# Performance work log

Hardware: AMD Instinct MI355X
Metric: run time of the kernel (lower is better)

Reference implementation:

```python
import jax, jax.numpy as jnp
import numpy as np

HEADS = 8
NEG_SLOPE = 0.2  # PyG GATConv default LeakyReLU slope


def _gat_layer(x, src, dst, W, a_src, a_dst, bias, heads, out_ch):
    """PyG-style GATConv (concat heads, self-loops already appended, eval mode).
    x: [N, F_in]; src/dst: [E_tot] int; W: [F_in, heads*out_ch];
    a_src/a_dst: [heads, out_ch]; bias: [heads*out_ch].
    """
    N = x.shape[0]
    h = (x @ W).reshape(N, heads, out_ch)                      # [N, H, C]
    # per-node attention logits (gathered per edge as scalars, not features)
    al_s = jnp.einsum('nhc,hc->nh', h, a_src)                  # [N, H]
    al_d = jnp.einsum('nhc,hc->nh', h, a_dst)                  # [N, H]
    e = jax.nn.leaky_relu(al_s[src] + al_d[dst], negative_slope=NEG_SLOPE)  # [E, H]
    # segment softmax over incoming edges of each target node (stable)
    e_max = jax.ops.segment_max(e, dst, num_segments=N)        # self-loops => no empty segments
    ex = jnp.exp(e - e_max[dst])
    denom = jax.ops.segment_sum(ex, dst, num_segments=N)
    alpha = ex / (denom[dst] + 1e-16)                          # [E, H]
    # gather source features, weight, scatter-add to targets
    out = jax.ops.segment_sum(h[src] * alpha[:, :, None], dst, num_segments=N)  # [N, H, C]
    return out.reshape(N, heads * out_ch) + bias


def setup_inputs() -> dict:
    key = jax.random.key(0)
    ks = jax.random.split(key, 16)
    N, E, F_IN, NUM_CLASSES = 50000, 1600000, 128, 16
    s = 0.1
    return {
        'x': jax.random.normal(ks[0], (N, F_IN), dtype=jnp.float32),
        'edge_index': jax.random.randint(ks[1], (2, E), 0, N, dtype=jnp.int64),
        # GAT layer 1: 128 -> 8 heads x 8
        'W1': jax.random.normal(ks[2], (F_IN, 64), dtype=jnp.float32) * s,
        'a1_src': jax.random.normal(ks[3], (8, 8), dtype=jnp.float32) * s,
        'a1_dst': jax.random.normal(ks[4], (8, 8), dtype=jnp.float32) * s,
        'b1': jnp.zeros((64,), dtype=jnp.float32),
        # GAT layer 2: 64 -> 8 heads x 4
        'W2': jax.random.normal(ks[5], (64, 32), dtype=jnp.float32) * s,
        'a2_src': jax.random.normal(ks[6], (8, 4), dtype=jnp.float32) * s,
        'a2_dst': jax.random.normal(ks[7], (8, 4), dtype=jnp.float32) * s,
        'b2': jnp.zeros((32,), dtype=jnp.float32),
        # torch MultiheadAttention(32, 8): packed in_proj [96,32], out_proj [32,32]
        'in_proj_w': jax.random.normal(ks[8], (96, 32), dtype=jnp.float32) * s,
        'in_proj_b': jnp.zeros((96,), dtype=jnp.float32),
        'out_proj_w': jax.random.normal(ks[9], (32, 32), dtype=jnp.float32) * s,
        'out_proj_b': jnp.zeros((32,), dtype=jnp.float32),
        # fc: 32 -> num_classes
        'fc_w': jax.random.normal(ks[10], (NUM_CLASSES, 32), dtype=jnp.float32) * s,
        'fc_b': jnp.zeros((NUM_CLASSES,), dtype=jnp.float32),
    }


def reference(x, edge_index, W1, a1_src, a1_dst, b1, W2, a2_src, a2_dst, b2,
              in_proj_w, in_proj_b, out_proj_w, out_proj_b, fc_w, fc_b):
    N = x.shape[0]
    loops = jnp.arange(N, dtype=edge_index.dtype)
    src = jnp.concatenate([edge_index[0], loops])  # PyG add_self_loops=True
    dst = jnp.concatenate([edge_index[1], loops])

    h = jax.nn.elu(_gat_layer(x, src, dst, W1, a1_src, a1_dst, b1, HEADS, 8))   # [N, 64]
    h = jax.nn.elu(_gat_layer(h, src, dst, W2, a2_src, a2_dst, b2, HEADS, 4))   # [N, 32]

    # MultiheadAttention on h.unsqueeze(0): shape [1, N, 32] with torch's
    # seq-first layout => seq_len = 1, batch = N. Softmax over a single key
    # is identically 1 for every head, so out = out_proj(v_proj(h)).
    v = h @ in_proj_w[64:96].T + in_proj_b[64:96]   # v-projection slice of packed in_proj
    h = v @ out_proj_w.T + out_proj_b               # [N, 32]

    logits = h @ fc_w.T + fc_b                      # [N, num_classes]
    return jax.nn.log_softmax(logits, axis=1)
```

## Files before the change

### kernel.cpp

```cpp
#include <hip/hip_runtime.h>
#include <hip/hip_bf16.h>
#include <math.h>


#define BSHIFT 7
#define BMASK  ((1 << BSHIFT) - 1)
#define MAXNB  512
#define TILE   8192
#define XST    136

typedef __attribute__((ext_vector_type(8))) short short8;
typedef __attribute__((ext_vector_type(4))) float floatx4;
typedef __attribute__((ext_vector_type(2))) float floatx2;

__device__ __forceinline__ unsigned short f2bf(float f) {
    union { float f; unsigned int u; } v; v.f = f;
    unsigned int u = v.u;
    return (unsigned short)((u + 0x7FFFu + ((u >> 16) & 1u)) >> 16);
}
__device__ __forceinline__ float lrelu(float e) { return fmaxf(e, 0.2f * e); }
__device__ __forceinline__ float elu(float o) {
    return (o > 0.f) ? o : (__expf(o) - 1.f);
}

__global__ __launch_bounds__(256) void bin_scatter1_kernel(
    const int* __restrict__ ei, int E, int Et, int NB, int CAP,
    int* __restrict__ gcount, unsigned int* __restrict__ rec) {
    __shared__ int h[MAXNB];
    __shared__ int cur[MAXNB];
    for (int i = threadIdx.x; i < NB; i += 256) h[i] = 0;
    __syncthreads();
    int tile0 = blockIdx.x * TILE;
    int jend = tile0 + TILE; if (jend > Et) jend = Et;
    for (int j = tile0 + threadIdx.x; j < jend; j += 256) {
        int d = (j < E) ? ei[E + j] : (j - E);
        atomicAdd(&h[d >> BSHIFT], 1);
    }
    __syncthreads();
    for (int i = threadIdx.x; i < NB; i += 256)
        cur[i] = h[i] ? atomicAdd(&gcount[i], h[i]) : 0;
    __syncthreads();
    for (int j = tile0 + threadIdx.x; j < jend; j += 256) {
        int srcv, d;
        if (j < E) { srcv = ei[j]; d = ei[E + j]; } else { srcv = j - E; d = j - E; }
        int b = d >> BSHIFT;
        int pos = atomicAdd(&cur[b], 1);
        if (pos < CAP)
            rec[(size_t)b * CAP + pos] = (unsigned)srcv | ((unsigned)(d & BMASK) << 16);
    }
}

__global__ __launch_bounds__(512) void scan_fold_kernel(
    const int* __restrict__ gcount, int* __restrict__ bbase, int NB, int CAP,
    const float* __restrict__ in_proj_w, const float* __restrict__ in_proj_b,
    const float* __restrict__ out_proj_w, const float* __restrict__ out_proj_b,
    const float* __restrict__ fc_w, const float* __restrict__ fc_b,
    float* __restrict__ M, float* __restrict__ bf) {
    __shared__ int s[512];
    __shared__ float Wvo[32 * 32];
    __shared__ float bvo[32];
    int t = threadIdx.x;
    if (blockIdx.x == 0) {
        int v = 0;
        if (t < NB) { v = gcount[t]; if (v > CAP) v = CAP; }
        s[t] = v;
        __syncthreads();
        for (int off = 1; off < 512; off <<= 1) {
            int u = (t >= off) ? s[t - off] : 0;
            __syncthreads();
            s[t] += u;
            __syncthreads();
        }
        if (t < NB) bbase[t] = s[t] - v;
    } else {
        const float* Wv = in_proj_w + 64 * 32;
        const float* bv = in_proj_b + 64;
        for (int idx = t; idx < 1024; idx += 512) {
            int i = idx >> 5, j = idx & 31;
            float acc = 0.f;
            for (int k = 0; k < 32; ++k) acc += out_proj_w[i * 32 + k] * Wv[k * 32 + j];
            Wvo[idx] = acc;
        }
        if (t < 32) {
            float acc = 0.f;
            for (int k = 0; k < 32; ++k) acc += out_proj_w[t * 32 + k] * bv[k];
            bvo[t] = acc + out_proj_b[t];
        }
        __syncthreads();
        for (int idx = t; idx < 16 * 32; idx += 512) {
            int cc = idx >> 5, j = idx & 31;
            float acc = 0.f;
            for (int i = 0; i < 32; ++i) acc += fc_w[cc * 32 + i] * Wvo[i * 32 + j];
            M[idx] = acc;
        }
        if (t < 16) {
            float acc = 0.f;
            for (int i = 0; i < 32; ++i) acc += fc_w[t * 32 + i] * bvo[i];
            bf[t] = acc + fc_b[t];
        }
    }
}

__global__ __launch_bounds__(256) void csr_finalize_kernel(
    const unsigned int* __restrict__ rec, const int* __restrict__ gcount,
    const int* __restrict__ bbase, int* __restrict__ rowp,
    unsigned short* __restrict__ esrc, int N, int Et, int CAP) {
    __shared__ int h[128];
    __shared__ int nb[128];
    __shared__ int cur[128];
    int b = blockIdx.x, t = threadIdx.x;
    size_t rbase = (size_t)b * CAP;
    int cnt = gcount[b]; if (cnt > CAP) cnt = CAP;
    int obase = bbase[b];
    if (t < 128) h[t] = 0;
    __syncthreads();
    for (int i = t; i < cnt; i += 256)
        atomicAdd(&h[(rec[rbase + i] >> 16) & 127], 1);
    __syncthreads();
    if (t == 0) {
        int run = obase;
        for (int i = 0; i < 128; ++i) { nb[i] = run; run += h[i]; }
    }
    __syncthreads();
    if (t < 128) cur[t] = nb[t];
    int n0 = b << BSHIFT;
    if (t < 128 && n0 + t < N) rowp[n0 + t] = nb[t];
    if (b == 0 && t == 0) rowp[N] = Et;
    __syncthreads();
    for (int i = t; i < cnt; i += 256) {
        unsigned r = rec[rbase + i];
        int pos = atomicAdd(&cur[(r >> 16) & 127], 1);
        esrc[pos] = (unsigned short)(r & 0xFFFFu);
    }
}

__global__ __launch_bounds__(256) void gemm1_mfma_kernel(
    const float* __restrict__ x, const float* __restrict__ W,
    const float* __restrict__ a_src, const float* __restrict__ a_dst,
    char* __restrict__ rec1, float* __restrict__ ald, int N) {
    __shared__ __align__(16) unsigned short xs[64 * XST];
    __shared__ __align__(16) unsigned short wt[64 * XST];
    int t = threadIdx.x;
    int nb = blockIdx.x * 64;
#pragma unroll
    for (int r = 0; r < 8; ++r) {
        int p = t + 256 * r;
        int row = p >> 5;
        int c4  = p & 31;
        int n = nb + row;
        float4 v = (n < N) ? ((const float4*)x)[(size_t)n * 32 + c4]
                           : make_float4(0.f, 0.f, 0.f, 0.f);
        unsigned short* dst = &xs[row * XST + c4 * 4];
        dst[0] = f2bf(v.x); dst[1] = f2bf(v.y);
        dst[2] = f2bf(v.z); dst[3] = f2bf(v.w);
    }
    {
        int n = t & 63, kg = t >> 6;
#pragma unroll
        for (int c = 0; c < 4; ++c) {
            int k0 = kg * 32 + c * 8;
            unsigned short* dst = &wt[n * XST + k0];
#pragma unroll
            for (int j = 0; j < 8; ++j)
                dst[j] = f2bf(W[(k0 + j) * 64 + n]);
        }
    }
    __syncthreads();
    int wave = t >> 6, lane = t & 63;
    int m16 = lane & 15, quad = lane >> 4;
    floatx4 acc[4];
#pragma unroll
    for (int i = 0; i < 4; ++i) acc[i] = (floatx4){0.f, 0.f, 0.f, 0.f};
#pragma unroll
    for (int k = 0; k < 4; ++k) {
        int koff = k * 32 + quad * 8;
        short8 afrag = *(const short8*)&xs[(wave * 16 + m16) * XST + koff];
#pragma unroll
        for (int nt = 0; nt < 4; ++nt) {
            short8 bfrag = *(const short8*)&wt[(nt * 16 + m16) * XST + koff];
            acc[nt] = __builtin_amdgcn_mfma_f32_16x16x32_bf16(afrag, bfrag, acc[nt], 0, 0, 0);
        }
    }
    __syncthreads();
    float* hs = (float*)xs;
#pragma unroll
    for (int nt = 0; nt < 4; ++nt)
#pragma unroll
        for (int r = 0; r < 4; ++r)
            hs[(wave * 16 + quad * 4 + r) * 65 + nt * 16 + m16] = acc[nt][r];
    __syncthreads();
    float asv = a_src[lane], adv = a_dst[lane];
    for (int itn = 0; itn < 16; ++itn) {
        int nl = wave * 16 + itn;
        int n = nb + nl;
        if (n >= N) break;
        float v = hs[nl * 65 + lane];
        float ps = v * asv, pd = v * adv;
        ps += __shfl_xor(ps, 1); ps += __shfl_xor(ps, 2); ps += __shfl_xor(ps, 4);
        pd += __shfl_xor(pd, 1); pd += __shfl_xor(pd, 2); pd += __shfl_xor(pd, 4);
        if ((lane & 7) == 0) {
            *(float*)(rec1 + (size_t)n * 96 + 4 * (lane >> 3)) = ps;
            ald[n * 8 + (lane >> 3)] = pd;
        }
        if (lane < 16) {
            const float* hr = &hs[nl * 65 + lane * 4];
            int pk = __builtin_amdgcn_cvt_pk_fp8_f32(hr[0], hr[1], 0, false);
            pk = __builtin_amdgcn_cvt_pk_fp8_f32(hr[2], hr[3], pk, true);
            *(unsigned*)(rec1 + (size_t)n * 96 + 32 + 4 * lane) = (unsigned)pk;
        }
    }
}

__global__ __launch_bounds__(256) void gat_agg64_g2_kernel(
    const int* __restrict__ rowp, const unsigned short* __restrict__ esrc,
    const char* __restrict__ rec1, const float* __restrict__ ald_arr,
    const float* __restrict__ bias,
    const float* __restrict__ W2, const float* __restrict__ a2s,
    const float* __restrict__ a2d,
    char* __restrict__ rec2, float* __restrict__ ald2, int N) {
    __shared__ __align__(16) float W2p[2][8][32][4];
    __shared__ __align__(16) float oL[4][64];
    __shared__ __align__(16) float h2L[4][32];
    int t = threadIdx.x;
    for (int idx = t; idx < 2048; idx += 256) {
        int k = idx >> 5, l = idx & 31;
        W2p[k >> 5][(k & 31) >> 2][l][k & 3] = W2[idx];
    }
    __syncthreads();
    const int lane = t & 63;
    const int wv = t >> 6;
    const int e = lane >> 4;
    const int c = lane & 15;
    const int hd = c >> 1;
    const int aoff = 4 * hd;
    const int foff = 32 + 4 * c;
    int n = blockIdx.x * 4 + wv;
    if (n >= N) return;
    float aldv = ald_arr[n * 8 + hd];
    int beg = rowp[n], end = rowp[n + 1];
    float dA = 0.f, dB = 0.f;
    floatx2 p0a = {0.f, 0.f}, p0b = {0.f, 0.f};
    floatx2 p1a = {0.f, 0.f}, p1b = {0.f, 0.f};
    floatx2 p2a = {0.f, 0.f}, p2b = {0.f, 0.f};
    floatx2 p3a = {0.f, 0.f}, p3b = {0.f, 0.f};
    int i = beg;
    int s0, s1, s2, s3;
    bool has = (i + 16 <= end);
    if (has) {
        s0 = esrc[i + e]; s1 = esrc[i + 4 + e];
        s2 = esrc[i + 8 + e]; s3 = esrc[i + 12 + e];
    }
    while (has) {
        int t0 = s0, t1 = s1, t2 = s2, t3 = s3;
        i += 16;
        has = (i + 16 <= end);
        if (has) {
            s0 = esrc[i + e]; s1 = esrc[i + 4 + e];
            s2 = esrc[i + 8 + e]; s3 = esrc[i + 12 + e];
        }
        const char* r0 = rec1 + (size_t)t0 * 96;
        const char* r1 = rec1 + (size_t)t1 * 96;
        const char* r2 = rec1 + (size_t)t2 * 96;
        const char* r3 = rec1 + (size_t)t3 * 96;
        float e0 = *(const float*)(r0 + aoff) + aldv;
        float e1 = *(const float*)(r1 + aoff) + aldv;
        float e2 = *(const float*)(r2 + aoff) + aldv;
        float e3 = *(const float*)(r3 + aoff) + aldv;
        unsigned g0 = *(const unsigned*)(r0 + foff);
        unsigned g1 = *(const unsigned*)(r1 + foff);
        unsigned g2 = *(const unsigned*)(r2 + foff);
        unsigned g3 = *(const unsigned*)(r3 + foff);
        float w0 = __expf(lrelu(e0));
        float w1 = __expf(lrelu(e1));
        float w2 = __expf(lrelu(e2));
        float w3 = __expf(lrelu(e3));
        dA += w0; dB += w1; dA += w2; dB += w3;
        p0a += w0 * __builtin_amdgcn_cvt_pk_f32_fp8(g0, false);
        p0b += w0 * __builtin_amdgcn_cvt_pk_f32_fp8(g0, true);
        p1a += w1 * __builtin_amdgcn_cvt_pk_f32_fp8(g1, false);
        p1b += w1 * __builtin_amdgcn_cvt_pk_f32_fp8(g1, true);
        p2a += w2 * __builtin_amdgcn_cvt_pk_f32_fp8(g2, false);
        p2b += w2 * __builtin_amdgcn_cvt_pk_f32_fp8(g2, true);
        p3a += w3 * __builtin_amdgcn_cvt_pk_f32_fp8(g3, false);
        p3b += w3 * __builtin_amdgcn_cvt_pk_f32_fp8(g3, true);
    }
    for (; i < end; i += 4) {
        int rem = end - i;
        int ee = (e < rem) ? e : rem - 1;
        int s = esrc[i + ee];
        const char* r = rec1 + (size_t)s * 96;
        float ev = *(const float*)(r + aoff) + aldv;
        unsigned g = *(const unsigned*)(r + foff);
        float w = (e < rem) ? __expf(lrelu(ev)) : 0.f;
        dA += w;
        p0a += w * __builtin_amdgcn_cvt_pk_f32_fp8(g, false);
        p0b += w * __builtin_amdgcn_cvt_pk_f32_fp8(g, true);
    }
    float d = dA + dB;
    floatx2 Pa = (p0a + p1a) + (p2a + p3a);
    floatx2 Pb = (p0b + p1b) + (p2b + p3b);
    float P0 = Pa.x, P1 = Pa.y, P2 = Pb.x, P3 = Pb.y;
    d  += __shfl_xor(d, 16);  d  += __shfl_xor(d, 32);
    P0 += __shfl_xor(P0, 16); P0 += __shfl_xor(P0, 32);
    P1 += __shfl_xor(P1, 16); P1 += __shfl_xor(P1, 32);
    P2 += __shfl_xor(P2, 16); P2 += __shfl_xor(P2, 32);
    P3 += __shfl_xor(P3, 16); P3 += __shfl_xor(P3, 32);
    float inv = 1.f / (d + 1e-16f);
    float4 bv = ((const float4*)bias)[c];
    float o0 = elu(P0 * inv + bv.x);
    float o1 = elu(P1 * inv + bv.y);
    float o2 = elu(P2 * inv + bv.z);
    float o3 = elu(P3 * inv + bv.w);
    if (lane < 16) *(float4*)&oL[wv][c * 4] = make_float4(o0, o1, o2, o3);
    const int l = lane & 31, kh = lane >> 5;
    const float* orow = &oL[wv][kh * 32];
    float a0 = 0.f, a1 = 0.f, a2 = 0.f, a3 = 0.f;
#pragma unroll
    for (int g = 0; g < 8; ++g) {
        float4 ov = *(const float4*)&orow[g * 4];
        float4 wv4 = *(const float4*)&W2p[kh][g][l][0];
        a0 += ov.x * wv4.x; a1 += ov.y * wv4.y;
        a2 += ov.z * wv4.z; a3 += ov.w * wv4.w;
    }
    float acc = (a0 + a1) + (a2 + a3);
    acc += __shfl_xor(acc, 32);
    float ps = acc * a2s[l], pd = acc * a2d[l];
    ps += __shfl_xor(ps, 1); ps += __shfl_xor(ps, 2);
    pd += __shfl_xor(pd, 1); pd += __shfl_xor(pd, 2);
    if (lane < 32) {
        h2L[wv][l] = acc;
        if ((l & 3) == 0) {
            *(float*)(rec2 + (size_t)n * 64 + 4 * (l >> 2)) = ps;
            ald2[n * 8 + (l >> 2)] = pd;
        }
    }
    if (lane < 8) {
        const float* hr = &h2L[wv][lane * 4];
        int pk = __builtin_amdgcn_cvt_pk_fp8_f32(hr[0], hr[1], 0, false);
        pk = __builtin_amdgcn_cvt_pk_fp8_f32(hr[2], hr[3], pk, true);
        *(unsigned*)(rec2 + (size_t)n * 64 + 32 + 4 * lane) = (unsigned)pk;
    }
}

__global__ __launch_bounds__(256) void gat_agg32_fin_kernel(
    const int* __restrict__ rowp, const unsigned short* __restrict__ esrc,
    const char* __restrict__ rec2, const float* __restrict__ ald_arr,
    const float* __restrict__ bias,
    const float* __restrict__ M, const float* __restrict__ bf,
    float* __restrict__ out, int N) {
    __shared__ __align__(16) float Mp[8][16][4];
    __shared__ float bfs[16];
    __shared__ __align__(16) float oL[4][32];
    int t = threadIdx.x;
    for (int i = t; i < 512; i += 256) {
        int j = i >> 5, k = i & 31;
        Mp[k >> 2][j][k & 3] = M[i];
    }
    if (t < 16) bfs[t] = bf[t];
    __syncthreads();
    const int lane = t & 63;
    const int wv = t >> 6;
    const int e = lane >> 3;
    const int c = lane & 7;
    const int aoff = 4 * c;
    const int foff = 32 + 4 * c;
    int n = blockIdx.x * 4 + wv;
    if (n >= N) return;
    float aldv = ald_arr[n * 8 + c];
    int beg = rowp[n], end = rowp[n + 1];
    float d0 = 0.f, d1 = 0.f, d2 = 0.f, d3 = 0.f;
    floatx2 p0a = {0.f, 0.f}, p0b = {0.f, 0.f};
    floatx2 p1a = {0.f, 0.f}, p1b = {0.f, 0.f};
    floatx2 p2a = {0.f, 0.f}, p2b = {0.f, 0.f};
    floatx2 p3a = {0.f, 0.f}, p3b = {0.f, 0.f};
    for (int base = beg; base < end; base += 32) {
        int i0 = base + e;
        int i1 = base + 8 + e;
        int i2 = base + 16 + e;
        int i3 = base + 24 + e;
        bool v0 = i0 < end, v1 = i1 < end, v2 = i2 < end, v3 = i3 < end;
        int c0 = v0 ? i0 : beg;
        int c1 = v1 ? i1 : beg;
        int c2 = v2 ? i2 : beg;
        int c3 = v3 ? i3 : beg;
        int s0 = esrc[c0], s1 = esrc[c1], s2 = esrc[c2], s3 = esrc[c3];
        const char* r0 = rec2 + (size_t)s0 * 64;
        const char* r1 = rec2 + (size_t)s1 * 64;
        const char* r2 = rec2 + (size_t)s2 * 64;
        const char* r3 = rec2 + (size_t)s3 * 64;
        float e0 = *(const float*)(r0 + aoff) + aldv;
        float e1 = *(const float*)(r1 + aoff) + aldv;
        float e2 = *(const float*)(r2 + aoff) + aldv;
        float e3 = *(const float*)(r3 + aoff) + aldv;
        unsigned g0 = *(const unsigned*)(r0 + foff);
        unsigned g1 = *(const unsigned*)(r1 + foff);
        unsigned g2 = *(const unsigned*)(r2 + foff);
        unsigned g3 = *(const unsigned*)(r3 + foff);
        float w0 = v0 ? __expf(lrelu(e0)) : 0.f;
        float w1 = v1 ? __expf(lrelu(e1)) : 0.f;
        float w2 = v2 ? __expf(lrelu(e2)) : 0.f;
        float w3 = v3 ? __expf(lrelu(e3)) : 0.f;
        d0 += w0; d1 += w1; d2 += w2; d3 += w3;
        p0a += w0 * __builtin_amdgcn_cvt_pk_f32_fp8(g0, false);
        p0b += w0 * __builtin_amdgcn_cvt_pk_f32_fp8(g0, true);
        p1a += w1 * __builtin_amdgcn_cvt_pk_f32_fp8(g1, false);
        p1b += w1 * __builtin_amdgcn_cvt_pk_f32_fp8(g1, true);
        p2a += w2 * __builtin_amdgcn_cvt_pk_f32_fp8(g2, false);
        p2b += w2 * __builtin_amdgcn_cvt_pk_f32_fp8(g2, true);
        p3a += w3 * __builtin_amdgcn_cvt_pk_f32_fp8(g3, false);
        p3b += w3 * __builtin_amdgcn_cvt_pk_f32_fp8(g3, true);
    }
    float d = (d0 + d1) + (d2 + d3);
    floatx2 Pa = (p0a + p1a) + (p2a + p3a);
    floatx2 Pb = (p0b + p1b) + (p2b + p3b);
    float P0 = Pa.x, P1 = Pa.y, P2 = Pb.x, P3 = Pb.y;
    d  += __shfl_xor(d, 8);  d  += __shfl_xor(d, 16);  d  += __shfl_xor(d, 32);
    P0 += __shfl_xor(P0, 8); P0 += __shfl_xor(P0, 16); P0 += __shfl_xor(P0, 32);
    P1 += __shfl_xor(P1, 8); P1 += __shfl_xor(P1, 16); P1 += __shfl_xor(P1, 32);
    P2 += __shfl_xor(P2, 8); P2 += __shfl_xor(P2, 16); P2 += __shfl_xor(P2, 32);
    P3 += __shfl_xor(P3, 8); P3 += __shfl_xor(P3, 16); P3 += __shfl_xor(P3, 32);
    float inv = 1.f / (d + 1e-16f);
    float4 bv = ((const float4*)bias)[c];
    float o0 = elu(P0 * inv + bv.x);
    float o1 = elu(P1 * inv + bv.y);
    float o2 = elu(P2 * inv + bv.z);
    float o3 = elu(P3 * inv + bv.w);
    if (lane < 8) *(float4*)&oL[wv][c * 4] = make_float4(o0, o1, o2, o3);
    const int j = lane & 15;
    const float* orow = oL[wv];
    float a0 = 0.f, a1 = 0.f, a2 = 0.f, a3 = 0.f;
#pragma unroll
    for (int g = 0; g < 8; ++g) {
        float4 ov = *(const float4*)&orow[g * 4];
        float4 mv = *(const float4*)&Mp[g][j][0];
        a0 += ov.x * mv.x; a1 += ov.y * mv.y;
        a2 += ov.z * mv.z; a3 += ov.w * mv.w;
    }
    float logit = (a0 + a1) + (a2 + a3) + bfs[j];
    float mx = logit;
    mx = fmaxf(mx, __shfl_xor(mx, 1));
    mx = fmaxf(mx, __shfl_xor(mx, 2));
    mx = fmaxf(mx, __shfl_xor(mx, 4));
    mx = fmaxf(mx, __shfl_xor(mx, 8));
    float ex = __expf(logit - mx);
    float se = ex;
    se += __shfl_xor(se, 1);
    se += __shfl_xor(se, 2);
    se += __shfl_xor(se, 4);
    se += __shfl_xor(se, 8);
    float res = logit - (mx + __logf(se));
    if (lane < 16) out[(size_t)n * 16 + j] = res;
}

extern "C" void kernel_launch(void* const* d_in, const int* in_sizes, int n_in,
                              void* d_out, int out_size, void* d_ws, size_t ws_size,
                              hipStream_t stream) {
    const float* x   = (const float*)d_in[0];
    const int*   ei  = (const int*)d_in[1];
    const float* W1  = (const float*)d_in[2];
    const float* a1s = (const float*)d_in[3];
    const float* a1d = (const float*)d_in[4];
    const float* b1  = (const float*)d_in[5];
    const float* W2  = (const float*)d_in[6];
    const float* a2s = (const float*)d_in[7];
    const float* a2d = (const float*)d_in[8];
    const float* b2  = (const float*)d_in[9];
    const float* ipw = (const float*)d_in[10];
    const float* ipb = (const float*)d_in[11];
    const float* opw = (const float*)d_in[12];
    const float* opb = (const float*)d_in[13];
    const float* fcw = (const float*)d_in[14];
    const float* fcb = (const float*)d_in[15];
    float* out = (float*)d_out;

    int N = in_sizes[0] / 128;
    int E = in_sizes[1] / 2;
    int Et = E + N;
    int NB = (N + BMASK) >> BSHIFT;
    int NTILES = (Et + TILE - 1) / TILE;
    int CAP = Et / NB;
    CAP = CAP + CAP / 8 + 256;
    CAP = (CAP + 255) & ~255;

    char* ws = (char*)d_ws;
    size_t off = 0;
    auto alloc = [&](size_t bytes) -> void* {
        void* p = ws + off;
        off += bytes;
        off = (off + 255) & ~(size_t)255;
        return p;
    };
    int*   bcount = (int*)alloc(MAXNB * 4);
    int*   bbase  = (int*)alloc(MAXNB * 4);
    unsigned int*   rec  = (unsigned int*)alloc((size_t)NB * CAP * 4);
    int*   rowp   = (int*)alloc((size_t)(N + 1) * 4);
    unsigned short* esrc = (unsigned short*)alloc((size_t)Et * 2);
    char* rec1   = (char*)alloc((size_t)N * 96);
    float* al1d  = (float*)alloc((size_t)N * 8 * 4);
    char* rec2   = (char*)alloc((size_t)N * 64);
    float* al2d  = (float*)alloc((size_t)N * 8 * 4);
    float* Mf    = (float*)alloc(512 * 4);
    float* bff   = (float*)alloc(16 * 4);
    (void)ws_size; (void)n_in; (void)out_size;

    hipMemsetAsync(bcount, 0, MAXNB * 4, stream);
    bin_scatter1_kernel<<<NTILES, 256, 0, stream>>>(ei, E, Et, NB, CAP, bcount, rec);
    scan_fold_kernel<<<2, 512, 0, stream>>>(bcount, bbase, NB, CAP,
                                            ipw, ipb, opw, opb, fcw, fcb, Mf, bff);
    csr_finalize_kernel<<<NB, 256, 0, stream>>>(rec, bcount, bbase, rowp, esrc, N, Et, CAP);

    gemm1_mfma_kernel<<<(N + 63) / 64, 256, 0, stream>>>(x, W1, a1s, a1d, rec1, al1d, N);
    gat_agg64_g2_kernel<<<(N + 3) / 4, 256, 0, stream>>>(
        rowp, esrc, rec1, al1d, b1, W2, a2s, a2d, rec2, al2d, N);
    gat_agg32_fin_kernel<<<(N + 3) / 4, 256, 0, stream>>>(
        rowp, esrc, rec2, al2d, b2, Mf, bff, out, N);
}
```

Baseline: 238.2 us.

## Stage edges in LDS, split layer-1 records, unroll aggregation loops

The binning kernel now caches each tile's packed (src,dst) edges in shared memory, so the second pass no longer rereads edge_index from global memory. Layer-1 per-node data is split from one 96-byte record into separate fp8 feature and source-logit arrays. The layer-1 aggregation loop is unrolled to 8 edges per lane with a masked tail, replacing the software-pipelined 4-edge loop. Layer-2 aggregation gains a mask-free fast path for full 32-edge chunks. The split layout reads two cache lines per gathered source instead of one, which may add memory traffic.

```diff
diff --git a/kernel.cpp b/kernel.cpp
--- a/kernel.cpp
+++ b/kernel.cpp
@@ -26,27 +26,32 @@
 __global__ __launch_bounds__(256) void bin_scatter1_kernel(
     const int* __restrict__ ei, int E, int Et, int NB, int CAP,
     int* __restrict__ gcount, unsigned int* __restrict__ rec) {
+    __shared__ unsigned int lrec[TILE];
     __shared__ int h[MAXNB];
     __shared__ int cur[MAXNB];
-    for (int i = threadIdx.x; i < NB; i += 256) h[i] = 0;
-    __syncthreads();
+    int t = threadIdx.x;
+    for (int i = t; i < NB; i += 256) h[i] = 0;
     int tile0 = blockIdx.x * TILE;
-    int jend = tile0 + TILE; if (jend > Et) jend = Et;
-    for (int j = tile0 + threadIdx.x; j < jend; j += 256) {
-        int d = (j < E) ? ei[E + j] : (j - E);
+    int cnt = Et - tile0; if (cnt > TILE) cnt = TILE;
+    __syncthreads();
+    for (int j = t; j < cnt; j += 256) {
+        int jj = tile0 + j;
+        int srcv, d;
+        if (jj < E) { srcv = ei[jj]; d = ei[E + jj]; } else { srcv = jj - E; d = jj - E; }
+        lrec[j] = (unsigned)srcv | ((unsigned)d << 16);
         atomicAdd(&h[d >> BSHIFT], 1);
     }
     __syncthreads();
-    for (int i = threadIdx.x; i < NB; i += 256)
+    for (int i = t; i < NB; i += 256)
         cur[i] = h[i] ? atomicAdd(&gcount[i], h[i]) : 0;
     __syncthreads();
-    for (int j = tile0 + threadIdx.x; j < jend; j += 256) {
-        int srcv, d;
-        if (j < E) { srcv = ei[j]; d = ei[E + j]; } else { srcv = j - E; d = j - E; }
-        int b = d >> BSHIFT;
+    for (int j = t; j < cnt; j += 256) {
+        unsigned v = lrec[j];
+        int b = v >> (16 + BSHIFT);
         int pos = atomicAdd(&cur[b], 1);
         if (pos < CAP)
-            rec[(size_t)b * CAP + pos] = (unsigned)srcv | ((unsigned)(d & BMASK) << 16);
+            rec[(size_t)b * CAP + pos] =
+                (v & 0xFFFFu) | ((((v >> 16) & BMASK)) << 16);
     }
 }
 
@@ -137,7 +142,8 @@
 __global__ __launch_bounds__(256) void gemm1_mfma_kernel(
     const float* __restrict__ x, const float* __restrict__ W,
     const float* __restrict__ a_src, const float* __restrict__ a_dst,
-    char* __restrict__ rec1, float* __restrict__ ald, int N) {
+    unsigned int* __restrict__ h1p, float* __restrict__ als,
+    float* __restrict__ ald, int N) {
     __shared__ __align__(16) unsigned short xs[64 * XST];
     __shared__ __align__(16) unsigned short wt[64 * XST];
     int t = threadIdx.x;
@@ -199,22 +205,22 @@
         ps += __shfl_xor(ps, 1); ps += __shfl_xor(ps, 2); ps += __shfl_xor(ps, 4);
         pd += __shfl_xor(pd, 1); pd += __shfl_xor(pd, 2); pd += __shfl_xor(pd, 4);
         if ((lane & 7) == 0) {
-            *(float*)(rec1 + (size_t)n * 96 + 4 * (lane >> 3)) = ps;
+            als[n * 8 + (lane >> 3)] = ps;
             ald[n * 8 + (lane >> 3)] = pd;
         }
         if (lane < 16) {
             const float* hr = &hs[nl * 65 + lane * 4];
             int pk = __builtin_amdgcn_cvt_pk_fp8_f32(hr[0], hr[1], 0, false);
             pk = __builtin_amdgcn_cvt_pk_fp8_f32(hr[2], hr[3], pk, true);
-            *(unsigned*)(rec1 + (size_t)n * 96 + 32 + 4 * lane) = (unsigned)pk;
+            h1p[(size_t)n * 16 + lane] = (unsigned)pk;
         }
     }
 }
 
 __global__ __launch_bounds__(256) void gat_agg64_g2_kernel(
     const int* __restrict__ rowp, const unsigned short* __restrict__ esrc,
-    const char* __restrict__ rec1, const float* __restrict__ ald_arr,
-    const float* __restrict__ bias,
+    const unsigned int* __restrict__ feat, const float* __restrict__ als,
+    const float* __restrict__ ald_arr, const float* __restrict__ bias,
     const float* __restrict__ W2, const float* __restrict__ a2s,
     const float* __restrict__ a2d,
     char* __restrict__ rec2, float* __restrict__ ald2, int N) {
@@ -232,8 +238,6 @@
     const int e = lane >> 4;
     const int c = lane & 15;
     const int hd = c >> 1;
-    const int aoff = 4 * hd;
-    const int foff = 32 + 4 * c;
     int n = blockIdx.x * 4 + wv;
     if (n >= N) return;
     float aldv = ald_arr[n * 8 + hd];
@@ -244,37 +248,29 @@
     floatx2 p2a = {0.f, 0.f}, p2b = {0.f, 0.f};
     floatx2 p3a = {0.f, 0.f}, p3b = {0.f, 0.f};
     int i = beg;
-    int s0, s1, s2, s3;
-    bool has = (i + 16 <= end);
-    if (has) {
-        s0 = esrc[i + e]; s1 = esrc[i + 4 + e];
-        s2 = esrc[i + 8 + e]; s3 = esrc[i + 12 + e];
-    }
-    while (has) {
-        int t0 = s0, t1 = s1, t2 = s2, t3 = s3;
-        i += 16;
-        has = (i + 16 <= end);
-        if (has) {
-            s0 = esrc[i + e]; s1 = esrc[i + 4 + e];
-            s2 = esrc[i + 8 + e]; s3 = esrc[i + 12 + e];
-        }
-        const char* r0 = rec1 + (size_t)t0 * 96;
-        const char* r1 = rec1 + (size_t)t1 * 96;
-        const char* r2 = rec1 + (size_t)t2 * 96;
-        const char* r3 = rec1 + (size_t)t3 * 96;
-        float e0 = *(const float*)(r0 + aoff) + aldv;
-        float e1 = *(const float*)(r1 + aoff) + aldv;
-        float e2 = *(const float*)(r2 + aoff) + aldv;
-        float e3 = *(const float*)(r3 + aoff) + aldv;
-        unsigned g0 = *(const unsigned*)(r0 + foff);
-        unsigned g1 = *(const unsigned*)(r1 + foff);
-        unsigned g2 = *(const unsigned*)(r2 + foff);
-        unsigned g3 = *(const unsigned*)(r3 + foff);
-        float w0 = __expf(lrelu(e0));
-        float w1 = __expf(lrelu(e1));
-        float w2 = __expf(lrelu(e2));
-        float w3 = __expf(lrelu(e3));
-        dA += w0; dB += w1; dA += w2; dB += w3;
+    for (; i + 32 <= end; i += 32) {
+        int s0 = esrc[i + e],      s1 = esrc[i + 4 + e];
+        int s2 = esrc[i + 8 + e],  s3 = esrc[i + 12 + e];
+        int s4 = esrc[i + 16 + e], s5 = esrc[i + 20 + e];
+        int s6 = esrc[i + 24 + e], s7 = esrc[i + 28 + e];
+        float e0 = als[s0 * 8 + hd], e1 = als[s1 * 8 + hd];
+        float e2 = als[s2 * 8 + hd], e3 = als[s3 * 8 + hd];
+        float e4 = als[s4 * 8 + hd], e5 = als[s5 * 8 + hd];
+        float e6 = als[s6 * 8 + hd], e7 = als[s7 * 8 + hd];
+        unsigned g0 = feat[s0 * 16 + c], g1 = feat[s1 * 16 + c];
+        unsigned g2 = feat[s2 * 16 + c], g3 = feat[s3 * 16 + c];
+        unsigned g4 = feat[s4 * 16 + c], g5 = feat[s5 * 16 + c];
+        unsigned g6 = feat[s6 * 16 + c], g7 = feat[s7 * 16 + c];
+        float w0 = __expf(lrelu(e0 + aldv));
+        float w1 = __expf(lrelu(e1 + aldv));
+        float w2 = __expf(lrelu(e2 + aldv));
+        float w3 = __expf(lrelu(e3 + aldv));
+        float w4 = __expf(lrelu(e4 + aldv));
+        float w5 = __expf(lrelu(e5 + aldv));
+        float w6 = __expf(lrelu(e6 + aldv));
+        float w7 = __expf(lrelu(e7 + aldv));
+        dA += w0 + w2; dB += w1 + w3;
+        dA += w4 + w6; dB += w5 + w7;
         p0a += w0 * __builtin_amdgcn_cvt_pk_f32_fp8(g0, false);
         p0b += w0 * __builtin_amdgcn_cvt_pk_f32_fp8(g0, true);
         p1a += w1 * __builtin_amdgcn_cvt_pk_f32_fp8(g1, false);
@@ -283,18 +279,40 @@
         p2b += w2 * __builtin_amdgcn_cvt_pk_f32_fp8(g2, true);
         p3a += w3 * __builtin_amdgcn_cvt_pk_f32_fp8(g3, false);
         p3b += w3 * __builtin_amdgcn_cvt_pk_f32_fp8(g3, true);
-    }
-    for (; i < end; i += 4) {
-        int rem = end - i;
-        int ee = (e < rem) ? e : rem - 1;
-        int s = esrc[i + ee];
-        const char* r = rec1 + (size_t)s * 96;
-        float ev = *(const float*)(r + aoff) + aldv;
-        unsigned g = *(const unsigned*)(r + foff);
-        float w = (e < rem) ? __expf(lrelu(ev)) : 0.f;
-        dA += w;
-        p0a += w * __builtin_amdgcn_cvt_pk_f32_fp8(g, false);
-        p0b += w * __builtin_amdgcn_cvt_pk_f32_fp8(g, true);
+        p0a += w4 * __builtin_amdgcn_cvt_pk_f32_fp8(g4, false);
+        p0b += w4 * __builtin_amdgcn_cvt_pk_f32_fp8(g4, true);
+        p1a += w5 * __builtin_amdgcn_cvt_pk_f32_fp8(g5, false);
+        p1b += w5 * __builtin_amdgcn_cvt_pk_f32_fp8(g5, true);
+        p2a += w6 * __builtin_amdgcn_cvt_pk_f32_fp8(g6, false);
+        p2b += w6 * __builtin_amdgcn_cvt_pk_f32_fp8(g6, true);
+        p3a += w7 * __builtin_amdgcn_cvt_pk_f32_fp8(g7, false);
+        p3b += w7 * __builtin_amdgcn_cvt_pk_f32_fp8(g7, true);
+    }
+    for (; i < end; i += 16) {
+        int i0 = i + e, i1 = i + 4 + e, i2 = i + 8 + e, i3 = i + 12 + e;
+        bool v0 = i0 < end, v1 = i1 < end, v2 = i2 < end, v3 = i3 < end;
+        int c0 = v0 ? i0 : beg;
+        int c1 = v1 ? i1 : beg;
+        int c2 = v2 ? i2 : beg;
+        int c3 = v3 ? i3 : beg;
+        int s0 = esrc[c0], s1 = esrc[c1], s2 = esrc[c2], s3 = esrc[c3];
+        float e0 = als[s0 * 8 + hd], e1 = als[s1 * 8 + hd];
+        float e2 = als[s2 * 8 + hd], e3 = als[s3 * 8 + hd];
+        unsigned g0 = feat[s0 * 16 + c], g1 = feat[s1 * 16 + c];
+        unsigned g2 = feat[s2 * 16 + c], g3 = feat[s3 * 16 + c];
+        float w0 = v0 ? __expf(lrelu(e0 + aldv)) : 0.f;
+        float w1 = v1 ? __expf(lrelu(e1 + aldv)) : 0.f;
+        float w2 = v2 ? __expf(lrelu(e2 + aldv)) : 0.f;
+        float w3 = v3 ? __expf(lrelu(e3 + aldv)) : 0.f;
+        dA += w0 + w2; dB += w1 + w3;
+        p0a += w0 * __builtin_amdgcn_cvt_pk_f32_fp8(g0, false);
+        p0b += w0 * __builtin_amdgcn_cvt_pk_f32_fp8(g0, true);
+        p1a += w1 * __builtin_amdgcn_cvt_pk_f32_fp8(g1, false);
+        p1b += w1 * __builtin_amdgcn_cvt_pk_f32_fp8(g1, true);
+        p2a += w2 * __builtin_amdgcn_cvt_pk_f32_fp8(g2, false);
+        p2b += w2 * __builtin_amdgcn_cvt_pk_f32_fp8(g2, true);
+        p3a += w3 * __builtin_amdgcn_cvt_pk_f32_fp8(g3, false);
+        p3b += w3 * __builtin_amdgcn_cvt_pk_f32_fp8(g3, true);
     }
     float d = dA + dB;
     floatx2 Pa = (p0a + p1a) + (p2a + p3a);
@@ -373,7 +391,37 @@
     floatx2 p1a = {0.f, 0.f}, p1b = {0.f, 0.f};
     floatx2 p2a = {0.f, 0.f}, p2b = {0.f, 0.f};
     floatx2 p3a = {0.f, 0.f}, p3b = {0.f, 0.f};
-    for (int base = beg; base < end; base += 32) {
+    int base = beg;
+    for (; base + 32 <= end; base += 32) {
+        int s0 = esrc[base + e],      s1 = esrc[base + 8 + e];
+        int s2 = esrc[base + 16 + e], s3 = esrc[base + 24 + e];
+        const char* r0 = rec2 + (size_t)s0 * 64;
+        const char* r1 = rec2 + (size_t)s1 * 64;
+        const char* r2 = rec2 + (size_t)s2 * 64;
+        const char* r3 = rec2 + (size_t)s3 * 64;
+        float e0 = *(const float*)(r0 + aoff) + aldv;
+        float e1 = *(const float*)(r1 + aoff) + aldv;
+        float e2 = *(const float*)(r2 + aoff) + aldv;
+        float e3 = *(const float*)(r3 + aoff) + aldv;
+        unsigned g0 = *(const unsigned*)(r0 + foff);
+        unsigned g1 = *(const unsigned*)(r1 + foff);
+        unsigned g2 = *(const unsigned*)(r2 + foff);
+        unsigned g3 = *(const unsigned*)(r3 + foff);
+        float w0 = __expf(lrelu(e0));
+        float w1 = __expf(lrelu(e1));
+        float w2 = __expf(lrelu(e2));
+        float w3 = __expf(lrelu(e3));
+        d0 += w0; d1 += w1; d2 += w2; d3 += w3;
+        p0a += w0 * __builtin_amdgcn_cvt_pk_f32_fp8(g0, false);
+        p0b += w0 * __builtin_amdgcn_cvt_pk_f32_fp8(g0, true);
+        p1a += w1 * __builtin_amdgcn_cvt_pk_f32_fp8(g1, false);
+        p1b += w1 * __builtin_amdgcn_cvt_pk_f32_fp8(g1, true);
+        p2a += w2 * __builtin_amdgcn_cvt_pk_f32_fp8(g2, false);
+        p2b += w2 * __builtin_amdgcn_cvt_pk_f32_fp8(g2, true);
+        p3a += w3 * __builtin_amdgcn_cvt_pk_f32_fp8(g3, false);
+        p3b += w3 * __builtin_amdgcn_cvt_pk_f32_fp8(g3, true);
+    }
+    for (; base < end; base += 32) {
         int i0 = base + e;
         int i1 = base + 8 + e;
         int i2 = base + 16 + e;
@@ -495,7 +543,8 @@
     unsigned int*   rec  = (unsigned int*)alloc((size_t)NB * CAP * 4);
     int*   rowp   = (int*)alloc((size_t)(N + 1) * 4);
     unsigned short* esrc = (unsigned short*)alloc((size_t)Et * 2);
-    char* rec1   = (char*)alloc((size_t)N * 96);
+    unsigned int* h1p = (unsigned int*)alloc((size_t)N * 16 * 4);
+    float* al1s  = (float*)alloc((size_t)N * 8 * 4);
     float* al1d  = (float*)alloc((size_t)N * 8 * 4);
     char* rec2   = (char*)alloc((size_t)N * 64);
     float* al2d  = (float*)alloc((size_t)N * 8 * 4);
@@ -509,9 +558,9 @@
                                             ipw, ipb, opw, opb, fcw, fcb, Mf, bff);
     csr_finalize_kernel<<<NB, 256, 0, stream>>>(rec, bcount, bbase, rowp, esrc, N, Et, CAP);
 
-    gemm1_mfma_kernel<<<(N + 63) / 64, 256, 0, stream>>>(x, W1, a1s, a1d, rec1, al1d, N);
+    gemm1_mfma_kernel<<<(N + 63) / 64, 256, 0, stream>>>(x, W1, a1s, a1d, h1p, al1s, al1d, N);
     gat_agg64_g2_kernel<<<(N + 3) / 4, 256, 0, stream>>>(
-        rowp, esrc, rec1, al1d, b1, W2, a2s, a2d, rec2, al2d, N);
+        rowp, esrc, h1p, al1s, al1d, b1, W2, a2s, a2d, rec2, al2d, N);
     gat_agg32_fin_kernel<<<(N + 3) / 4, 256, 0, stream>>>(
         rowp, esrc, rec2, al2d, b2, Mf, bff, out, N);
 }
```

Result: faster. 230.7 us (-3.2%).
